# Optimization experiments

Hardware: AMD Instinct MI355X
Metric: run time of the kernel (lower is better)

Reference implementation:

```python
import jax, jax.numpy as jnp
import numpy as np

B, C_LEN, Q_LEN, D = 8, 2048, 512, 1024


def setup_inputs() -> dict:
    key = jax.random.key(0)
    ks = jax.random.split(key, 10)
    scale = 1.0 / np.sqrt(D)
    return {
        "c": jax.random.normal(ks[0], (B, C_LEN, D), dtype=jnp.float32),
        "q": jax.random.normal(ks[1], (B, Q_LEN, D), dtype=jnp.float32),
        "w_cq": jax.random.normal(ks[2], (D,), dtype=jnp.float32) * scale,
        "b_cq": jax.random.normal(ks[3], (), dtype=jnp.float32) * scale,
        "w_c": jax.random.normal(ks[4], (D,), dtype=jnp.float32) * scale,
        "b_c": jax.random.normal(ks[5], (), dtype=jnp.float32) * scale,
        "w_q": jax.random.normal(ks[6], (D,), dtype=jnp.float32) * scale,
        "b_q": jax.random.normal(ks[7], (), dtype=jnp.float32) * scale,
        "W_l": jax.random.normal(ks[8], (D, 4 * D), dtype=jnp.float32) * (1.0 / np.sqrt(4 * D)),
        "b_l": jax.random.normal(ks[9], (D,), dtype=jnp.float32) * (1.0 / np.sqrt(4 * D)),
    }


def reference(c, q, w_cq, b_cq, w_c, b_c, w_q, b_q, W_l, b_l):
    # trilinear term: the original loops over q positions computing
    # att_weight_cq(c * q_i); since that Linear is rank-1, this is one einsum.
    cq = jnp.einsum('bcd,bqd,d->bcq', c, q, w_cq) + b_cq        # [B, C, Q]
    s = (c @ w_c + b_c)[:, :, None] + (q @ w_q + b_q)[:, None, :] + cq
    a = jax.nn.softmax(s, axis=2)                               # c2q attention
    c2q_att = jnp.einsum('bcq,bqd->bcd', a, q)                  # [B, C, D]
    b_att = jax.nn.softmax(jnp.max(s, axis=2), axis=1)          # [B, C]
    q2c_att = jnp.einsum('bc,bcd->bd', b_att, c)[:, None, :]    # [B, 1, D]
    x = jnp.concatenate([c, c2q_att, c * c2q_att, c * q2c_att], axis=-1)
    z = x @ W_l.T + b_l                                         # [B, C, D]
    return z
```

## Files before the change

### kernel.cpp

```cpp
#include <hip/hip_runtime.h>

typedef unsigned short u16;
typedef __attribute__((ext_vector_type(4))) float floatx4;
typedef __attribute__((ext_vector_type(4))) unsigned short u16x4;
typedef __attribute__((ext_vector_type(8))) short short8;
typedef __attribute__((ext_vector_type(8))) __bf16 bf16x8;

#define B_SZ 8
#define C_LEN 2048
#define Q_LEN 512
#define D_DIM 1024
#define K4 (4 * D_DIM)

static __device__ __forceinline__ u16 f2bf(float f) {
    union { float f; unsigned int u; } v; v.f = f;
    unsigned int r = v.u + 0x7FFFu + ((v.u >> 16) & 1u);
    return (u16)(r >> 16);
}
static __device__ __forceinline__ float bf2f(u16 h) {
    union { unsigned int u; float f; } v; v.u = ((unsigned int)h) << 16;
    return v.f;
}

static __device__ __forceinline__ void async16(const void* g, void* l) {
    __builtin_amdgcn_global_load_lds(
        (const __attribute__((address_space(1))) unsigned int*)g,
        (__attribute__((address_space(3))) unsigned int*)(unsigned int)(unsigned long long)l,
        16, 0, 0);
}

__global__ __launch_bounds__(256) void prep_kernel(
    const float* __restrict__ c, const float* __restrict__ q,
    const float* __restrict__ w_cq, const float* __restrict__ w_c, const float* __restrict__ w_q,
    u16* __restrict__ cbf, u16* __restrict__ qwbf, u16* __restrict__ qT,
    float* __restrict__ rowterm, float* __restrict__ colterm, float* __restrict__ q2c) {
    int blk = blockIdx.x;
    int tid = threadIdx.x;
    if (blk < 4096) {
        int row = blk * 4 + (tid >> 6);
        int lane = tid & 63;
        const float* src = c + (size_t)row * D_DIM;
        u16* dst = cbf + (size_t)row * D_DIM;
        float s = 0.f;
        #pragma unroll
        for (int j = 0; j < 4; ++j) {
            int idx = j * 256 + lane * 4;
            floatx4 a = *(const floatx4*)(src + idx);
            floatx4 w = *(const floatx4*)(w_c + idx);
            s += a[0]*w[0] + a[1]*w[1] + a[2]*w[2] + a[3]*w[3];
            u16x4 o;
            #pragma unroll
            for (int e = 0; e < 4; ++e) o[e] = f2bf(a[e]);
            *(u16x4*)(dst + idx) = o;
        }
        for (int off = 32; off; off >>= 1) s += __shfl_down(s, off);
        if (lane == 0) rowterm[row] = s;
    } else if (blk < 5120) {
        int row = (blk - 4096) * 4 + (tid >> 6);
        int lane = tid & 63;
        const float* src = q + (size_t)row * D_DIM;
        u16* dst = qwbf + (size_t)row * D_DIM;
        float s = 0.f;
        #pragma unroll
        for (int j = 0; j < 4; ++j) {
            int idx = j * 256 + lane * 4;
            floatx4 a  = *(const floatx4*)(src + idx);
            floatx4 wc = *(const floatx4*)(w_cq + idx);
            floatx4 wq = *(const floatx4*)(w_q + idx);
            s += a[0]*wq[0] + a[1]*wq[1] + a[2]*wq[2] + a[3]*wq[3];
            u16x4 o;
            #pragma unroll
            for (int e = 0; e < 4; ++e) o[e] = f2bf(a[e] * wc[e]);
            *(u16x4*)(dst + idx) = o;
        }
        for (int off = 32; off; off >>= 1) s += __shfl_down(s, off);
        if (lane == 0) colterm[row] = s;
    } else if (blk < 9216) {
        __shared__ float tile[32][33];
        int t = blk - 5120;
        int q0 = (t & 15) * 32;
        int d0 = ((t >> 4) & 31) * 32;
        int b = t >> 9;
        int tx = tid & 31, ty = tid >> 5;
        const float* qb = q + (size_t)b * Q_LEN * D_DIM;
        #pragma unroll
        for (int j = 0; j < 4; ++j) {
            int row = ty + j * 8;
            tile[row][tx] = qb[(size_t)(q0 + row) * D_DIM + d0 + tx];
        }
        __syncthreads();
        u16* qTb = qT + (size_t)b * D_DIM * Q_LEN;
        #pragma unroll
        for (int j = 0; j < 4; ++j) {
            int row = ty + j * 8;
            qTb[(size_t)(d0 + row) * Q_LEN + q0 + tx] = f2bf(tile[tx][row]);
        }
    } else {
        int i = (blk - 9216) * 256 + tid;
        q2c[i] = 0.0f;
    }
}

__global__ __launch_bounds__(256) void wmerge_all(const float* __restrict__ W, const float* __restrict__ q2c,
                                                  u16* __restrict__ Wm, u16* __restrict__ Wbf) {
    int n = blockIdx.x;
    int k = threadIdx.x * 4;
    const float* wr = W + (size_t)n * K4;
    floatx4 w1 = *(const floatx4*)(wr + k);
    floatx4 w4 = *(const floatx4*)(wr + 3072 + k);
    #pragma unroll
    for (int p = 0; p < 2; ++p) {
        int kk = p * 1024 + k;
        floatx4 v = *(const floatx4*)(wr + 1024 + kk);
        u16x4 o;
        #pragma unroll
        for (int e = 0; e < 4; ++e) o[e] = f2bf(v[e]);
        *(u16x4*)(Wbf + (size_t)n * 2048 + kk) = o;
    }
    #pragma unroll
    for (int b = 0; b < 8; ++b) {
        floatx4 g = *(const floatx4*)(q2c + (size_t)b * D_DIM + k);
        u16x4 o;
        #pragma unroll
        for (int e = 0; e < 4; ++e) o[e] = f2bf(w1[e] + w4[e] * g[e]);
        *(u16x4*)(Wm + (size_t)b * 1048576 + (size_t)n * 1024 + k) = o;
    }
}

template<int MODE>
__global__ __launch_bounds__(256) void gemm_async(
    const u16* __restrict__ A0, const u16* __restrict__ A1, const u16* __restrict__ A2,
    const u16* __restrict__ B0, const u16* __restrict__ B1,
    float* __restrict__ of, u16* __restrict__ ob, const float* __restrict__ bias) {
    constexpr int NSEC = (MODE == 2) ? 3 : 1;
    constexpr int KSEC = (MODE == 1) ? 512 : 1024;
    constexpr int LDO  = (MODE == 0) ? 512 : 1024;
    constexpr int NTILES = (MODE == 0) ? 4 : 8;
    __shared__ u16 As[128 * 64];
    __shared__ u16 Bs[128 * 64];
    const int tid  = threadIdx.x;
    const int lane = tid & 63;
    const int wave = tid >> 6;
    const int lin  = blockIdx.x;
    const int b    = lin & 7;
    const int rem  = lin >> 3;
    const int n0   = (rem % NTILES) * 128;
    const int m0   = (rem / NTILES) * 128;

    const u16* Aarr[NSEC];
    const u16* Barr[NSEC];
    int lda_[NSEC], ldb_[NSEC];
    if constexpr (MODE == 0) {
        Aarr[0] = A0 + (size_t)b * C_LEN * D_DIM; lda_[0] = 1024;
        Barr[0] = B0 + (size_t)b * Q_LEN * D_DIM; ldb_[0] = 1024;
    } else if constexpr (MODE == 1) {
        Aarr[0] = A0 + (size_t)b * C_LEN * Q_LEN; lda_[0] = 512;
        Barr[0] = B0 + (size_t)b * D_DIM * Q_LEN; ldb_[0] = 512;
    } else {
        Aarr[0] = A0 + (size_t)b * C_LEN * D_DIM;  lda_[0] = 1024;
        Barr[0] = B0 + (size_t)b * D_DIM * D_DIM;  ldb_[0] = 1024;
        Aarr[1] = A1 + (size_t)b * C_LEN * 2048;        lda_[1] = 2048;
        Barr[1] = B1;                                   ldb_[1] = 2048;
        Aarr[2] = A1 + (size_t)b * C_LEN * 2048 + 1024; lda_[2] = 2048;
        Barr[2] = B1 + 1024;                            ldb_[2] = 2048;
    }

    const int srow = lane >> 3;
    const int ssc  = ((lane & 7) ^ srow) * 8;

    floatx4 acc[4][4];
    #pragma unroll
    for (int i = 0; i < 4; ++i)
        #pragma unroll
        for (int j = 0; j < 4; ++j)
            acc[i][j] = (floatx4)(0.0f);

    const int wrow = (wave >> 1) * 64;
    const int wcol = (wave & 1) * 64;
    const int quad = lane >> 4;
    const int lrow = lane & 15;
    const int sw7  = lane & 7;

    #pragma unroll
    for (int sec = 0; sec < NSEC; ++sec) {
        const u16* __restrict__ Ab = Aarr[sec];
        const u16* __restrict__ Bb = Barr[sec];
        const int LA = lda_[sec];
        const int LB = ldb_[sec];
        for (int k0 = 0; k0 < KSEC; k0 += 64) {
            #pragma unroll
            for (int cc = 0; cc < 4; ++cc) {
                int ch = wave * 4 + cc;
                int rr = ch * 8 + srow;
                async16(Ab + (size_t)(m0 + rr) * LA + k0 + ssc, &As[ch * 512]);
            }
            #pragma unroll
            for (int cc = 0; cc < 4; ++cc) {
                int ch = wave * 4 + cc;
                int rr = ch * 8 + srow;
                async16(Bb + (size_t)(n0 + rr) * LB + k0 + ssc, &Bs[ch * 512]);
            }
            __syncthreads();
            #pragma unroll
            for (int h = 0; h < 2; ++h) {
                const int pc = ((h * 4 + quad) ^ sw7) * 8;
                bf16x8 af[4], bfr[4];
                #pragma unroll
                for (int i = 0; i < 4; ++i)
                    af[i] = __builtin_bit_cast(bf16x8, *(const short8*)&As[(wrow + i*16 + lrow) * 64 + pc]);
                #pragma unroll
                for (int j = 0; j < 4; ++j)
                    bfr[j] = __builtin_bit_cast(bf16x8, *(const short8*)&Bs[(wcol + j*16 + lrow) * 64 + pc]);
                #pragma unroll
                for (int i = 0; i < 4; ++i)
                    #pragma unroll
                    for (int j = 0; j < 4; ++j)
                        acc[i][j] = __builtin_amdgcn_mfma_f32_16x16x32_bf16(af[i], bfr[j], acc[i][j], 0, 0, 0);
            }
            __syncthreads();
        }
    }

    float* ofb = nullptr; u16* ccb = nullptr; const u16* cbr = nullptr;
    if (MODE == 0)      ofb = of + (size_t)b * C_LEN * Q_LEN;
    else if (MODE == 1) { ccb = ob + (size_t)b * C_LEN * 2048; cbr = A1 + (size_t)b * C_LEN * D_DIM; }
    else                ofb = of + (size_t)b * C_LEN * D_DIM;
    #pragma unroll
    for (int i = 0; i < 4; ++i) {
        #pragma unroll
        for (int j = 0; j < 4; ++j) {
            #pragma unroll
            for (int e = 0; e < 4; ++e) {
                int gm = m0 + wrow + i * 16 + quad * 4 + e;
                int gn = n0 + wcol + j * 16 + lrow;
                float v = acc[i][j][e];
                if (MODE == 0)      ofb[(size_t)gm * LDO + gn] = v;
                else if (MODE == 1) {
                    u16 p = f2bf(v);
                    float cv = bf2f(cbr[(size_t)gm * 1024 + gn]);
                    ccb[(size_t)gm * 2048 + gn]        = p;
                    ccb[(size_t)gm * 2048 + 1024 + gn] = f2bf(cv * bf2f(p));
                }
                else                ofb[(size_t)gm * LDO + gn] = v + bias[gn];
            }
        }
    }
}

__global__ void softmax_kernel(const float* __restrict__ S, const float* __restrict__ colterm,
                               u16* __restrict__ P, float* __restrict__ mbuf) {
    int row = blockIdx.x * 4 + (threadIdx.x >> 6);
    int lane = threadIdx.x & 63;
    int b = row >> 11;
    const float* sp = S + (size_t)row * Q_LEN;
    const float* cp = colterm + (size_t)b * Q_LEN;
    float v[8];
    float m = -1e30f;
    #pragma unroll
    for (int j = 0; j < 8; ++j) {
        int idx = j * 64 + lane;
        v[j] = sp[idx] + cp[idx];
        m = fmaxf(m, v[j]);
    }
    for (int off = 32; off; off >>= 1) m = fmaxf(m, __shfl_xor(m, off));
    float s = 0.f;
    #pragma unroll
    for (int j = 0; j < 8; ++j) { v[j] = __expf(v[j] - m); s += v[j]; }
    for (int off = 32; off; off >>= 1) s += __shfl_xor(s, off);
    float inv = 1.0f / s;
    u16* pp = P + (size_t)row * Q_LEN;
    #pragma unroll
    for (int j = 0; j < 8; ++j) pp[j * 64 + lane] = f2bf(v[j] * inv);
    if (lane == 0) mbuf[row] = m;
}

__global__ __launch_bounds__(256) void batt_kernel(const float* __restrict__ mbuf,
                                                   const float* __restrict__ rowterm,
                                                   float* __restrict__ batt) {
    __shared__ float red[8];
    int b = blockIdx.x;
    int tid = threadIdx.x;
    const float* mb = mbuf + (size_t)b * C_LEN;
    const float* rt = rowterm + (size_t)b * C_LEN;
    float v[8];
    float m = -1e30f;
    #pragma unroll
    for (int j = 0; j < 8; ++j) { int idx = j * 256 + tid; v[j] = mb[idx] + rt[idx]; m = fmaxf(m, v[j]); }
    for (int off = 32; off; off >>= 1) m = fmaxf(m, __shfl_xor(m, off));
    int wave = tid >> 6, lane = tid & 63;
    if (lane == 0) red[wave] = m;
    __syncthreads();
    m = fmaxf(fmaxf(red[0], red[1]), fmaxf(red[2], red[3]));
    float s = 0.f;
    #pragma unroll
    for (int j = 0; j < 8; ++j) { v[j] = __expf(v[j] - m); s += v[j]; }
    for (int off = 32; off; off >>= 1) s += __shfl_xor(s, off);
    if (lane == 0) red[4 + wave] = s;
    __syncthreads();
    s = red[4] + red[5] + red[6] + red[7];
    float inv = 1.0f / s;
    float* bb = batt + (size_t)b * C_LEN;
    #pragma unroll
    for (int j = 0; j < 8; ++j) bb[j * 256 + tid] = v[j] * inv;
}

__global__ __launch_bounds__(256) void q2c_kernel(const float* __restrict__ batt,
                                                  const u16* __restrict__ cbf,
                                                  float* __restrict__ q2c) {
    int d  = blockIdx.x * 256 + threadIdx.x;
    int b  = blockIdx.y;
    int c0 = blockIdx.z * 256;
    const u16* cb = cbf + ((size_t)b * C_LEN + c0) * D_DIM + d;
    const float* bb = batt + (size_t)b * C_LEN + c0;
    float s = 0.f;
    #pragma unroll 4
    for (int i = 0; i < 256; ++i) s += bb[i] * bf2f(cb[(size_t)i * D_DIM]);
    atomicAdd(&q2c[(size_t)b * D_DIM + d], s);
}

extern "C" void kernel_launch(void* const* d_in, const int* in_sizes, int n_in,
                              void* d_out, int out_size, void* d_ws, size_t ws_size,
                              hipStream_t stream) {
    const float* c   = (const float*)d_in[0];
    const float* q   = (const float*)d_in[1];
    const float* wcq = (const float*)d_in[2];
    const float* w_c = (const float*)d_in[4];
    const float* w_q = (const float*)d_in[6];
    const float* W_l = (const float*)d_in[8];
    const float* b_l = (const float*)d_in[9];
    float* out = (float*)d_out;

    char* ws = (char*)d_ws;
    u16*   cbf     = (u16*)ws;
    float* S       = (float*)(ws + 33554432);
    u16*   CC      = (u16*)(ws + 33554432);
    u16*   qwbf    = (u16*)(ws + 67108864);
    u16*   P       = (u16*)(ws + 100663296);
    u16*   Wm      = (u16*)(ws + 100663296);
    u16*   qT      = (u16*)(ws + 117440512);
    u16*   Wbf     = (u16*)(ws + 117440512);
    float* rowterm = (float*)(ws + 125829120);
    float* colterm = (float*)(ws + 125894656);
    float* mbuf    = (float*)(ws + 125911040);
    float* batt    = (float*)(ws + 125976576);
    float* q2c     = (float*)(ws + 126042112);

    prep_kernel<<<dim3(9248), dim3(256), 0, stream>>>(c, q, wcq, w_c, w_q,
                                                      cbf, qwbf, qT, rowterm, colterm, q2c);
    gemm_async<0><<<dim3(512), dim3(256), 0, stream>>>(cbf, nullptr, nullptr, qwbf, nullptr, S, nullptr, nullptr);
    softmax_kernel<<<dim3(4096), dim3(256), 0, stream>>>(S, colterm, P, mbuf);
    batt_kernel<<<dim3(8), dim3(256), 0, stream>>>(mbuf, rowterm, batt);
    q2c_kernel<<<dim3(4, 8, 8), dim3(256), 0, stream>>>(batt, cbf, q2c);
    gemm_async<1><<<dim3(1024), dim3(256), 0, stream>>>(P, cbf, nullptr, qT, nullptr, nullptr, CC, nullptr);
    wmerge_all<<<dim3(1024), dim3(256), 0, stream>>>(W_l, q2c, Wm, Wbf);
    gemm_async<2><<<dim3(1024), dim3(256), 0, stream>>>(cbf, CC, nullptr, Wm, Wbf, out, nullptr, b_l);
}
```

Measured before the change: 363.7 us.

## Replace final projection GEMM with 256x256-tile, 8-wave phased pipelined kernel

The final GEMM (c, c2q, c*c2q with merged weights, K=3072) now runs in a dedicated kernel. It uses 512-thread blocks computing 256x256 output tiles, a double-buffered LDS with half-K staging and explicit vmcnt waits, and an 8-phase schedule that interleaves LDS reads, async global loads and MFMA bursts at raised priority. The larger tiles give more data reuse per block and the schedule is meant to hide memory latency behind MFMA work. The cost is a grid of only 256 blocks, which may underfill the GPU, plus heavy register use and many barriers.

```diff
diff --git a/kernel.cpp b/kernel.cpp
--- a/kernel.cpp
+++ b/kernel.cpp
@@ -247,6 +247,139 @@
     }
 }
 
+#define PIN() __builtin_amdgcn_sched_barrier(0)
+#define BAR8() do { PIN(); __builtin_amdgcn_s_barrier(); PIN(); } while (0)
+#define VMW(N) do { asm volatile("s_waitcnt vmcnt(" #N ")" ::: "memory"); } while (0)
+
+#define LDA4(DST, MQ, KH, CUR) do { \
+    const u16* un_ = lds_ + (CUR) * 32768 + (KH) * 8192; \
+    _Pragma("unroll") \
+    for (int i_ = 0; i_ < 4; ++i_) \
+      (DST)[i_] = __builtin_bit_cast(bf16x8, \
+          *(const short8*)(un_ + (wm * 128 + (MQ) * 64 + i_ * 16 + lrow) * 32 + pcs)); \
+  } while (0)
+
+#define LDB4(DST, KH, CUR) do { \
+    const u16* un_ = lds_ + (CUR) * 32768 + 16384 + (KH) * 8192; \
+    _Pragma("unroll") \
+    for (int i_ = 0; i_ < 4; ++i_) \
+      (DST)[i_] = __builtin_bit_cast(bf16x8, \
+          *(const short8*)(un_ + (wn * 64 + i_ * 16 + lrow) * 32 + pcs)); \
+  } while (0)
+
+#define MFMA16(MQ4, A_, B_) do { \
+    __builtin_amdgcn_s_setprio(1); \
+    _Pragma("unroll") \
+    for (int i_ = 0; i_ < 4; ++i_) { \
+      _Pragma("unroll") \
+      for (int j_ = 0; j_ < 4; ++j_) \
+        acc[(MQ4) + i_][j_] = __builtin_amdgcn_mfma_f32_16x16x32_bf16( \
+            (A_)[i_], (B_)[j_], acc[(MQ4) + i_][j_], 0, 0, 0); \
+    } \
+    __builtin_amdgcn_s_setprio(0); \
+  } while (0)
+
+__global__ __launch_bounds__(512, 2) void gemm2_8ph(
+    const u16* __restrict__ cbf, const u16* __restrict__ CC,
+    const u16* __restrict__ Wm, const u16* __restrict__ Wbf,
+    float* __restrict__ of, const float* __restrict__ bias) {
+    __shared__ __align__(16) u16 lds_[65536];
+    const int tid  = threadIdx.x;
+    const int lane = tid & 63;
+    const int wave = tid >> 6;
+    const int lin  = blockIdx.x;
+    const int b    = lin & 7;
+    const int rem  = lin >> 3;
+    const int n0   = (rem & 3) * 256;
+    const int m0   = (rem >> 2) * 256;
+    const int wm   = wave >> 2;
+    const int wn   = wave & 3;
+    const int quad = lane >> 4;
+    const int lrow = lane & 15;
+    const int pcs  = (quad ^ (lrow & 3)) * 8;
+
+    const u16* Acb  = cbf + (size_t)b * (C_LEN * D_DIM);
+    const u16* Acc0 = CC  + (size_t)b * (C_LEN * 2048);
+    const u16* Acc1 = Acc0 + 1024;
+    const u16* Bwm  = Wm  + (size_t)b * (D_DIM * D_DIM);
+
+    auto STAGE = [&](int tt, int ab, int kh) {
+        const int sec = tt >> 4;
+        const int kl  = (tt & 15) * 64 + kh * 32;
+        const u16* base;
+        int r0;
+        if (ab == 0) { base = (sec == 0) ? Acb : (sec == 1) ? Acc0 : Acc1; r0 = m0; }
+        else         { base = (sec == 0) ? Bwm : (sec == 1) ? Wbf  : Wbf + 1024; r0 = n0; }
+        const int ld = (sec == 0) ? 1024 : 2048;
+        u16* unit = lds_ + (tt & 1) * 32768 + ab * 16384 + kh * 8192;
+        #pragma unroll
+        for (int l = 0; l < 2; ++l) {
+            const int li  = l * 512 + tid;
+            const int row = li >> 2;
+            const int sc  = (li & 3) ^ (row & 3);
+            async16(base + (size_t)(r0 + row) * ld + kl + sc * 8,
+                    unit + (l * 512 + (tid & ~63)) * 8);
+        }
+    };
+
+    floatx4 acc[8][4];
+    #pragma unroll
+    for (int i = 0; i < 8; ++i)
+        #pragma unroll
+        for (int j = 0; j < 4; ++j) acc[i][j] = (floatx4)(0.0f);
+
+    STAGE(0, 1, 0); PIN(); STAGE(0, 0, 0); PIN(); STAGE(0, 1, 1); PIN(); STAGE(0, 0, 1); PIN();
+    STAGE(1, 1, 0); PIN(); STAGE(1, 0, 0); PIN(); STAGE(1, 1, 1); PIN();
+    VMW(10);
+    BAR8();
+
+    bf16x8 af[4], bf[4];
+    for (int tt = 0; tt < 48; ++tt) {
+        const int cur = tt & 1;
+        if (tt + 1 < 48) STAGE(tt + 1, 0, 1);
+        LDA4(af, 0, 0, cur);
+        LDB4(bf, 0, cur);
+        BAR8();
+        MFMA16(0, af, bf);
+        BAR8();
+        if (tt + 2 < 48) STAGE(tt + 2, 1, 0);
+        LDA4(af, 1, 0, cur);
+        BAR8();
+        MFMA16(4, af, bf);
+        if (tt < 46) VMW(10); else VMW(0);
+        BAR8();
+        if (tt + 2 < 48) STAGE(tt + 2, 0, 0);
+        LDA4(af, 0, 1, cur);
+        LDB4(bf, 1, cur);
+        BAR8();
+        MFMA16(0, af, bf);
+        BAR8();
+        if (tt + 2 < 48) STAGE(tt + 2, 1, 1);
+        LDA4(af, 1, 1, cur);
+        BAR8();
+        MFMA16(4, af, bf);
+        if (tt < 46) VMW(10); else VMW(0);
+        BAR8();
+    }
+
+    float bs[4];
+    #pragma unroll
+    for (int j = 0; j < 4; ++j) bs[j] = bias[n0 + wn * 64 + j * 16 + lrow];
+    float* ofb = of + (size_t)b * (C_LEN * D_DIM);
+    #pragma unroll
+    for (int i = 0; i < 8; ++i) {
+        #pragma unroll
+        for (int j = 0; j < 4; ++j) {
+            #pragma unroll
+            for (int e = 0; e < 4; ++e) {
+                const int gm = m0 + wm * 128 + i * 16 + quad * 4 + e;
+                const int gn = n0 + wn * 64 + j * 16 + lrow;
+                ofb[(size_t)gm * D_DIM + gn] = acc[i][j][e] + bs[j];
+            }
+        }
+    }
+}
+
 __global__ void softmax_kernel(const float* __restrict__ S, const float* __restrict__ colterm,
                                u16* __restrict__ P, float* __restrict__ mbuf) {
     int row = blockIdx.x * 4 + (threadIdx.x >> 6);
@@ -353,5 +486,5 @@
     q2c_kernel<<<dim3(4, 8, 8), dim3(256), 0, stream>>>(batt, cbf, q2c);
     gemm_async<1><<<dim3(1024), dim3(256), 0, stream>>>(P, cbf, nullptr, qT, nullptr, nullptr, CC, nullptr);
     wmerge_all<<<dim3(1024), dim3(256), 0, stream>>>(W_l, q2c, Wm, Wbf);
-    gemm_async<2><<<dim3(1024), dim3(256), 0, stream>>>(cbf, CC, nullptr, Wm, Wbf, out, nullptr, b_l);
-}
+    gemm2_8ph<<<dim3(256), dim3(512), 0, stream>>>(cbf, CC, Wm, Wbf, out, b_l);
+}
```

New measurement: 358.0 us. Within noise of the previous version (-1.6%).
